# Kernel optimization log

Measured on AMD Instinct MI355X. Metric: run time of the kernel, lower is better.

Reference implementation:

```python
import jax, jax.numpy as jnp
import numpy as np

NUM_ITEMS = 10000
EMBED_DIM = 64
USER_PERSPECTIVE_IMPORTANCE = 0.5
LEAKY_SLOPE = 0.2
BATCH = 32
MAX_HIST = 200


def setup_inputs() -> dict:
    key = jax.random.key(0)
    k_ids, k_len, k_items, k_user, k_w, k_b = jax.random.split(key, 6)
    batch_history_ids = jax.random.randint(k_ids, (BATCH, MAX_HIST), 0, NUM_ITEMS, dtype=jnp.int32)
    # lengths must be >= 1 to avoid all-masked softmax rows
    batch_history_lengths = jnp.maximum(
        jax.random.randint(k_len, (BATCH,), 0, MAX_HIST, dtype=jnp.int32), 1)
    items_embedding = jax.random.normal(k_items, (NUM_ITEMS, EMBED_DIM), dtype=jnp.float32)
    user_embedding = jax.random.normal(k_user, (1, EMBED_DIM), dtype=jnp.float32)
    fc_weight = jax.random.normal(k_w, (EMBED_DIM, EMBED_DIM), dtype=jnp.float32) * (1.0 / np.sqrt(EMBED_DIM))
    fc_bias = jax.random.normal(k_b, (EMBED_DIM,), dtype=jnp.float32) * 0.01
    return {
        'batch_history_ids': batch_history_ids,
        'batch_history_lengths': batch_history_lengths,
        'items_embedding': items_embedding,
        'user_embedding': user_embedding,
        'fc_weight': fc_weight,
        'fc_bias': fc_bias,
    }


def reference(batch_history_ids, batch_history_lengths, items_embedding, user_embedding, fc_weight, fc_bias):
    # valid[b, n] = n < length[b]
    valid = jnp.arange(MAX_HIST)[None, :] < batch_history_lengths[:, None]  # [B, N]

    hist_emb = items_embedding[batch_history_ids]  # [B, N, F] ragged gather (padded)

    # item-perspective attention: [B, I, N]
    item_att = jnp.einsum('if,bnf->bin', items_embedding, hist_emb)
    # original adds -inf mask then leaky_relu; leaky_relu(-inf) = -inf -> softmax weight 0
    item_att = jnp.where(valid[:, None, :], jax.nn.leaky_relu(item_att, LEAKY_SLOPE), -jnp.inf)
    item_scores = jax.nn.softmax(item_att, axis=-1)  # [B, I, N]

    # user-perspective attention: constant across the item-query axis (q=1, repeated over I),
    # so compute once as [B, N] and broadcast (same math as 'qif,bnf->bqin').
    user_att = jnp.einsum('f,bnf->bn', user_embedding[0], hist_emb)
    user_att = jnp.where(valid, jax.nn.leaky_relu(user_att, LEAKY_SLOPE), -jnp.inf)
    user_scores = jax.nn.softmax(user_att, axis=-1)  # [B, N]

    w = USER_PERSPECTIVE_IMPORTANCE
    attn = (1.0 - w) * item_scores + w * user_scores[:, None, :]  # [B, I, N]

    personalized = jnp.einsum('bin,bnf->bif', attn, hist_emb)  # [B, I, F]
    projected = personalized @ fc_weight.T + fc_bias  # [B, I, F]
    # final per-item score: dot with item embedding
    return jnp.einsum('bif,if->bi', projected, items_embedding)  # [B, I]
```

## Files before the change

### kernel.cpp

```cpp
#include <hip/hip_runtime.h>
#include <hip/hip_bf16.h>
#include <math.h>

#define NUM_ITEMS 10000
#define EMBED_DIM 64
#define MAX_HIST 200
#define NPAD 208
#define BATCH 32
#define LEAKY 0.2f
#define W_USER 0.5f
#define LOG2E 1.4426950408889634f
#define M_INIT (-1e30f)

typedef short bf16x8 __attribute__((ext_vector_type(8)));
typedef float f32x4 __attribute__((ext_vector_type(4)));

__device__ __forceinline__ unsigned short f2bf(float f) {
    __hip_bfloat16 h = __float2bfloat16(f);
    return __builtin_bit_cast(unsigned short, h);
}

__device__ __forceinline__ float fexp2(float x) {
#if __has_builtin(__builtin_amdgcn_exp2f)
    return __builtin_amdgcn_exp2f(x);
#else
    return exp2f(x);
#endif
}

__global__ __launch_bounds__(256) void prep_kernel(const int* __restrict__ ids,
                                                   const int* __restrict__ lens,
                                                   const float* __restrict__ items,
                                                   const float* __restrict__ user,
                                                   const float* __restrict__ W,
                                                   const float* __restrict__ bias,
                                                   unsigned short* __restrict__ items_att_bf,
                                                   unsigned short* __restrict__ wti_bf,
                                                   float* __restrict__ bdot,
                                                   unsigned short* __restrict__ hist_bf,
                                                   float* __restrict__ us_ws) {
    const int tid = threadIdx.x;
    __shared__ float shW[EMBED_DIM * EMBED_DIM];
    __shared__ float red[8];

    if (blockIdx.x < NUM_ITEMS / 4) {
        for (int idx = tid; idx < EMBED_DIM * EMBED_DIM; idx += 256) shW[idx] = W[idx];
        __syncthreads();

        const int i = blockIdx.x * 4 + (tid >> 6);
        const int g = tid & 63;
        const float* irow = items + i * EMBED_DIM;

        float acc = 0.f;
#pragma unroll
        for (int f = 0; f < EMBED_DIM; ++f) acc += irow[f] * shW[f * EMBED_DIM + g];

        wti_bf[i * EMBED_DIM + g] = f2bf(acc);
        items_att_bf[i * EMBED_DIM + g] = f2bf(irow[g] * LOG2E);

        float bv = bias[g] * irow[g];
#pragma unroll
        for (int o = 32; o > 0; o >>= 1) bv += __shfl_xor(bv, o, 64);
        if (g == 0) bdot[i] = bv;
    } else {
        const int b = blockIdx.x - NUM_ITEMS / 4;

        for (int idx = tid; idx < NPAD * 8; idx += 256) {
            const int n = idx >> 3, q = idx & 7;
            bf16x8 v = (bf16x8)0;
            if (n < MAX_HIST) {
                const int id = ids[b * MAX_HIST + n];
                const float4* p = (const float4*)(items + id * EMBED_DIM + q * 8);
                float4 v0 = p[0], v1 = p[1];
                v[0] = (short)f2bf(v0.x); v[1] = (short)f2bf(v0.y);
                v[2] = (short)f2bf(v0.z); v[3] = (short)f2bf(v0.w);
                v[4] = (short)f2bf(v1.x); v[5] = (short)f2bf(v1.y);
                v[6] = (short)f2bf(v1.z); v[7] = (short)f2bf(v1.w);
            }
            *(bf16x8*)(hist_bf + (size_t)(b * NPAD + n) * EMBED_DIM + q * 8) = v;
        }

        const int len = lens[b];
        float s = -INFINITY;
        if (tid < len) {
            const int id = ids[b * MAX_HIST + tid];
            const float* h = items + id * EMBED_DIM;
            float a0 = 0.f, a1 = 0.f;
#pragma unroll
            for (int f = 0; f < EMBED_DIM; f += 2) {
                a0 += user[f] * h[f];
                a1 += user[f + 1] * h[f + 1];
            }
            float a = a0 + a1;
            s = fmaxf(a, LEAKY * a);
        }
        float m = s;
#pragma unroll
        for (int o = 32; o > 0; o >>= 1) m = fmaxf(m, __shfl_xor(m, o, 64));
        if ((tid & 63) == 0) red[tid >> 6] = m;
        __syncthreads();
        m = fmaxf(fmaxf(red[0], red[1]), fmaxf(red[2], red[3]));

        float e = (tid < len) ? __expf(s - m) : 0.f;
        float t = e;
#pragma unroll
        for (int o = 32; o > 0; o >>= 1) t += __shfl_xor(t, o, 64);
        if ((tid & 63) == 0) red[4 + (tid >> 6)] = t;
        __syncthreads();
        const float sum = red[4] + red[5] + red[6] + red[7];

        if (tid < NPAD) us_ws[b * NPAD + tid] = (tid < len) ? (e / sum) : 0.f;
    }
}

__global__ __launch_bounds__(256) void main_kernel(const unsigned short* __restrict__ items_att_bf,
                                                   const unsigned short* __restrict__ wti_bf,
                                                   const float* __restrict__ bdot,
                                                   const unsigned short* __restrict__ hist_bf,
                                                   const float* __restrict__ us_ws,
                                                   const int* __restrict__ lens,
                                                   float* __restrict__ out) {
    const int b = blockIdx.y;
    const int tid = threadIdx.x;
    const int lane = tid & 63;
    const int w = tid >> 6;

    __shared__ __align__(16) unsigned short sh_hist[NPAD * EMBED_DIM];
    __shared__ float sh_us[NPAD];

    const int len = lens[b];
    const int ntiles = (len + 15) >> 4;

    const float4* src = (const float4*)(hist_bf + (size_t)b * NPAD * EMBED_DIM);
    const int nf4 = ntiles * 16 * 8;
    for (int c = tid; c < nf4; c += 256) {
        const int n = c >> 3, q = c & 7;
        float4 v = src[c];
        const int byte = (n * 128 + q * 16) ^ ((n & 7) << 4);
        *(float4*)((char*)sh_hist + byte) = v;
    }
    for (int c = tid; c < ntiles * 16; c += 256) sh_us[c] = us_ws[b * NPAD + c];
    __syncthreads();

    const int i0 = blockIdx.x * 64 + w * 16;
    if (i0 >= NUM_ITEMS) return;

    const int c16 = lane & 15;
    const int g = lane >> 4;
    const int i = i0 + c16;

    bf16x8 itf0 = *(const bf16x8*)(items_att_bf + (size_t)i * 64 + g * 8);
    bf16x8 itf1 = *(const bf16x8*)(items_att_bf + (size_t)i * 64 + 32 + g * 8);
    bf16x8 wtf0 = *(const bf16x8*)(wti_bf + (size_t)i * 64 + g * 8);
    bf16x8 wtf1 = *(const bf16x8*)(wti_bf + (size_t)i * 64 + 32 + g * 8);

    float m = M_INIT, Se = 0.f, Sh = 0.f, Su = 0.f;

#define TILE_BODY(T, MASKED)                                                              \
    {                                                                                     \
        const int n = (T) * 16 + c16;                                                     \
        const int base = n * 128, sw = (n & 7) << 4;                                      \
        bf16x8 a0 = *(const bf16x8*)((const char*)sh_hist + ((base + g * 16) ^ sw));      \
        bf16x8 a1 = *(const bf16x8*)((const char*)sh_hist + ((base + 64 + g * 16) ^ sw)); \
        f32x4 S = (f32x4)0.f, H = (f32x4)0.f;                                             \
        S = __builtin_amdgcn_mfma_f32_16x16x32_bf16(a0, itf0, S, 0, 0, 0);                \
        S = __builtin_amdgcn_mfma_f32_16x16x32_bf16(a1, itf1, S, 0, 0, 0);                \
        H = __builtin_amdgcn_mfma_f32_16x16x32_bf16(a0, wtf0, H, 0, 0, 0);                \
        H = __builtin_amdgcn_mfma_f32_16x16x32_bf16(a1, wtf1, H, 0, 0, 0);                \
        const int nb = (T) * 16 + g * 4;                                                  \
        float s0 = fmaxf(S[0], LEAKY * S[0]);                                             \
        float s1 = fmaxf(S[1], LEAKY * S[1]);                                             \
        float s2 = fmaxf(S[2], LEAKY * S[2]);                                             \
        float s3 = fmaxf(S[3], LEAKY * S[3]);                                             \
        if (MASKED) {                                                                     \
            s0 = (nb + 0 < len) ? s0 : -INFINITY;                                         \
            s1 = (nb + 1 < len) ? s1 : -INFINITY;                                         \
            s2 = (nb + 2 < len) ? s2 : -INFINITY;                                         \
            s3 = (nb + 3 < len) ? s3 : -INFINITY;                                         \
        }                                                                                 \
        const float mn = fmaxf(fmaxf(fmaxf(s0, s1), fmaxf(s2, s3)), m);                   \
        const float cc = fexp2(m - mn);                                                   \
        const float e0 = fexp2(s0 - mn), e1 = fexp2(s1 - mn);                             \
        const float e2 = fexp2(s2 - mn), e3 = fexp2(s3 - mn);                             \
        const float4 usv = *(const float4*)(sh_us + (T) * 16 + g * 4);                    \
        Se = fmaf(Se, cc, (e0 + e1) + (e2 + e3));                                         \
        Sh = fmaf(Sh, cc, fmaf(e0, H[0], fmaf(e1, H[1], fmaf(e2, H[2], e3 * H[3]))));     \
        Su = fmaf(usv.x, H[0], fmaf(usv.y, H[1], fmaf(usv.z, H[2], fmaf(usv.w, H[3], Su)))); \
        m = mn;                                                                           \
    }

    for (int t = 0; t < ntiles - 1; ++t) TILE_BODY(t, 0)
    TILE_BODY(ntiles - 1, 1)
#undef TILE_BODY

#pragma unroll
    for (int off = 16; off <= 32; off <<= 1) {
        const float m2 = __shfl_xor(m, off, 64);
        const float Se2 = __shfl_xor(Se, off, 64);
        const float Sh2 = __shfl_xor(Sh, off, 64);
        const float mn = fmaxf(m, m2);
        const float c1 = fexp2(m - mn);
        const float c2 = fexp2(m2 - mn);
        Se = Se * c1 + Se2 * c2;
        Sh = Sh * c1 + Sh2 * c2;
        m = mn;
    }
    Su += __shfl_xor(Su, 16, 64);
    Su += __shfl_xor(Su, 32, 64);

    if (g == 0)
        out[(size_t)b * NUM_ITEMS + i] =
            (1.0f - W_USER) * (Sh / Se) + W_USER * Su + bdot[i];
}

extern "C" void kernel_launch(void* const* d_in, const int* in_sizes, int n_in,
                              void* d_out, int out_size, void* d_ws, size_t ws_size,
                              hipStream_t stream) {
    const int* ids = (const int*)d_in[0];
    const int* lens = (const int*)d_in[1];
    const float* items = (const float*)d_in[2];
    const float* user = (const float*)d_in[3];
    const float* W = (const float*)d_in[4];
    const float* bias = (const float*)d_in[5];
    float* out = (float*)d_out;

    char* p = (char*)d_ws;
    unsigned short* items_att_bf = (unsigned short*)p; p += (size_t)NUM_ITEMS * EMBED_DIM * 2;
    unsigned short* wti_bf       = (unsigned short*)p; p += (size_t)NUM_ITEMS * EMBED_DIM * 2;
    float* bdot                  = (float*)p;          p += (size_t)NUM_ITEMS * 4;
    unsigned short* hist_bf      = (unsigned short*)p; p += (size_t)BATCH * NPAD * EMBED_DIM * 2;
    float* us_ws                 = (float*)p;          p += (size_t)BATCH * NPAD * 4;

    prep_kernel<<<NUM_ITEMS / 4 + BATCH, 256, 0, stream>>>(ids, lens, items, user, W, bias,
                                                           items_att_bf, wti_bf, bdot,
                                                           hist_bf, us_ws);

    dim3 grid((NUM_ITEMS + 63) / 64, BATCH);
    main_kernel<<<grid, 256, 0, stream>>>(items_att_bf, wti_bf, bdot, hist_bf, us_ws, lens, out);
}
```

Baseline: 41.55 us.

## Precompute user-weighted history vector and drop online softmax max tracking

The user-perspective term is moved into the prep kernel: the user softmax weights are applied to the gathered history once per batch, producing a 64-dim bf16 vector. The main kernel then gets that term from two MFMAs against the item's projection row instead of accumulating it per tile. The item softmax also drops its running-max rescaling and exponentiates clamped scores directly, which removes the per-tile max and correction exp and the cross-lane max merge. In exchange it relies on scores staying within a clamped range where exp2 does not overflow, which changes numerics if scores exceed the clamp, and adds some serial gather work in prep.

Measured after the change: 45.76 us. 10.1% more time.

```diff
diff --git a/kernel.cpp b/kernel.cpp
--- a/kernel.cpp
+++ b/kernel.cpp
@@ -10,7 +10,7 @@
 #define LEAKY 0.2f
 #define W_USER 0.5f
 #define LOG2E 1.4426950408889634f
-#define M_INIT (-1e30f)
+#define ECLAMP 110.0f
 
 typedef short bf16x8 __attribute__((ext_vector_type(8)));
 typedef float f32x4 __attribute__((ext_vector_type(4)));
@@ -38,10 +38,12 @@
                                                    unsigned short* __restrict__ wti_bf,
                                                    float* __restrict__ bdot,
                                                    unsigned short* __restrict__ hist_bf,
-                                                   float* __restrict__ us_ws) {
+                                                   unsigned short* __restrict__ uh_bf) {
     const int tid = threadIdx.x;
     __shared__ float shW[EMBED_DIM * EMBED_DIM];
     __shared__ float red[8];
+    __shared__ float sh_usf[NPAD];
+    __shared__ float sh_uh[4][EMBED_DIM];
 
     if (blockIdx.x < NUM_ITEMS / 4) {
         for (int idx = tid; idx < EMBED_DIM * EMBED_DIM; idx += 256) shW[idx] = W[idx];
@@ -109,7 +111,19 @@
         __syncthreads();
         const float sum = red[4] + red[5] + red[6] + red[7];
 
-        if (tid < NPAD) us_ws[b * NPAD + tid] = (tid < len) ? (e / sum) : 0.f;
+        if (tid < NPAD) sh_usf[tid] = (tid < len) ? (e / sum) : 0.f;
+        __syncthreads();
+
+        const int f = tid & 63;
+        const int part = tid >> 6;
+        float uhp = 0.f;
+        for (int n = part; n < len; n += 4)
+            uhp += sh_usf[n] * items[(size_t)ids[b * MAX_HIST + n] * EMBED_DIM + f];
+        sh_uh[part][f] = uhp;
+        __syncthreads();
+        if (tid < EMBED_DIM)
+            uh_bf[b * EMBED_DIM + tid] =
+                f2bf(sh_uh[0][tid] + sh_uh[1][tid] + sh_uh[2][tid] + sh_uh[3][tid]);
     }
 }
 
@@ -117,7 +131,7 @@
                                                    const unsigned short* __restrict__ wti_bf,
                                                    const float* __restrict__ bdot,
                                                    const unsigned short* __restrict__ hist_bf,
-                                                   const float* __restrict__ us_ws,
+                                                   const unsigned short* __restrict__ uh_bf,
                                                    const int* __restrict__ lens,
                                                    float* __restrict__ out) {
     const int b = blockIdx.y;
@@ -126,7 +140,6 @@
     const int w = tid >> 6;
 
     __shared__ __align__(16) unsigned short sh_hist[NPAD * EMBED_DIM];
-    __shared__ float sh_us[NPAD];
 
     const int len = lens[b];
     const int ntiles = (len + 15) >> 4;
@@ -139,7 +152,6 @@
         const int byte = (n * 128 + q * 16) ^ ((n & 7) << 4);
         *(float4*)((char*)sh_hist + byte) = v;
     }
-    for (int c = tid; c < ntiles * 16; c += 256) sh_us[c] = us_ws[b * NPAD + c];
     __syncthreads();
 
     const int i0 = blockIdx.x * 64 + w * 16;
@@ -154,7 +166,14 @@
     bf16x8 wtf0 = *(const bf16x8*)(wti_bf + (size_t)i * 64 + g * 8);
     bf16x8 wtf1 = *(const bf16x8*)(wti_bf + (size_t)i * 64 + 32 + g * 8);
 
-    float m = M_INIT, Se = 0.f, Sh = 0.f, Su = 0.f;
+    bf16x8 u0 = *(const bf16x8*)(uh_bf + b * 64 + g * 8);
+    bf16x8 u1 = *(const bf16x8*)(uh_bf + b * 64 + 32 + g * 8);
+    f32x4 suf = (f32x4)0.f;
+    suf = __builtin_amdgcn_mfma_f32_16x16x32_bf16(u0, wtf0, suf, 0, 0, 0);
+    suf = __builtin_amdgcn_mfma_f32_16x16x32_bf16(u1, wtf1, suf, 0, 0, 0);
+    const float Su = suf[0];
+
+    float Se = 0.f, Sh = 0.f;
 
 #define TILE_BODY(T, MASKED)                                                              \
     {                                                                                     \
@@ -178,35 +197,18 @@
             s2 = (nb + 2 < len) ? s2 : -INFINITY;                                         \
             s3 = (nb + 3 < len) ? s3 : -INFINITY;                                         \
         }                                                                                 \
-        const float mn = fmaxf(fmaxf(fmaxf(s0, s1), fmaxf(s2, s3)), m);                   \
-        const float cc = fexp2(m - mn);                                                   \
-        const float e0 = fexp2(s0 - mn), e1 = fexp2(s1 - mn);                             \
-        const float e2 = fexp2(s2 - mn), e3 = fexp2(s3 - mn);                             \
-        const float4 usv = *(const float4*)(sh_us + (T) * 16 + g * 4);                    \
-        Se = fmaf(Se, cc, (e0 + e1) + (e2 + e3));                                         \
-        Sh = fmaf(Sh, cc, fmaf(e0, H[0], fmaf(e1, H[1], fmaf(e2, H[2], e3 * H[3]))));     \
-        Su = fmaf(usv.x, H[0], fmaf(usv.y, H[1], fmaf(usv.z, H[2], fmaf(usv.w, H[3], Su)))); \
-        m = mn;                                                                           \
+        const float e0 = fexp2(fminf(s0, ECLAMP)), e1 = fexp2(fminf(s1, ECLAMP));         \
+        const float e2 = fexp2(fminf(s2, ECLAMP)), e3 = fexp2(fminf(s3, ECLAMP));         \
+        Se += (e0 + e1) + (e2 + e3);                                                      \
+        Sh = fmaf(e0, H[0], fmaf(e1, H[1], fmaf(e2, H[2], fmaf(e3, H[3], Sh))));          \
     }
 
     for (int t = 0; t < ntiles - 1; ++t) TILE_BODY(t, 0)
     TILE_BODY(ntiles - 1, 1)
 #undef TILE_BODY
 
-#pragma unroll
-    for (int off = 16; off <= 32; off <<= 1) {
-        const float m2 = __shfl_xor(m, off, 64);
-        const float Se2 = __shfl_xor(Se, off, 64);
-        const float Sh2 = __shfl_xor(Sh, off, 64);
-        const float mn = fmaxf(m, m2);
-        const float c1 = fexp2(m - mn);
-        const float c2 = fexp2(m2 - mn);
-        Se = Se * c1 + Se2 * c2;
-        Sh = Sh * c1 + Sh2 * c2;
-        m = mn;
-    }
-    Su += __shfl_xor(Su, 16, 64);
-    Su += __shfl_xor(Su, 32, 64);
+    Se += __shfl_xor(Se, 16, 64); Se += __shfl_xor(Se, 32, 64);
+    Sh += __shfl_xor(Sh, 16, 64); Sh += __shfl_xor(Sh, 32, 64);
 
     if (g == 0)
         out[(size_t)b * NUM_ITEMS + i] =
@@ -229,12 +231,12 @@
     unsigned short* wti_bf       = (unsigned short*)p; p += (size_t)NUM_ITEMS * EMBED_DIM * 2;
     float* bdot                  = (float*)p;          p += (size_t)NUM_ITEMS * 4;
     unsigned short* hist_bf      = (unsigned short*)p; p += (size_t)BATCH * NPAD * EMBED_DIM * 2;
-    float* us_ws                 = (float*)p;          p += (size_t)BATCH * NPAD * 4;
+    unsigned short* uh_bf        = (unsigned short*)p; p += (size_t)BATCH * EMBED_DIM * 2;
 
     prep_kernel<<<NUM_ITEMS / 4 + BATCH, 256, 0, stream>>>(ids, lens, items, user, W, bias,
                                                            items_att_bf, wti_bf, bdot,
-                                                           hist_bf, us_ws);
+                                                           hist_bf, uh_bf);
 
     dim3 grid((NUM_ITEMS + 63) / 64, BATCH);
-    main_kernel<<<grid, 256, 0, stream>>>(items_att_bf, wti_bf, bdot, hist_bf, us_ws, lens, out);
-}
+    main_kernel<<<grid, 256, 0, stream>>>(items_att_bf, wti_bf, bdot, hist_bf, uh_bf, lens, out);
+}
```
